# Optimization experiments

Measured on AMD Instinct MI355X. Metric: run time of the kernel, lower is better.

## Reference

```python
import jax, jax.numpy as jnp
import numpy as np

B, T, L, W = 4, 4096, 64, 8          # batch, text len, media tokens, max_window_per_audio
DIM, DIM_A, H, DH = 2048, 1024, 8, 64
INNER = H * DH
LN_EPS = 1e-5


def setup_inputs() -> dict:
    key = jax.random.key(0)
    ks = jax.random.split(key, 8)
    x = jax.random.normal(ks[0], (B, T, DIM), jnp.float32)
    media = jax.random.normal(ks[1], (B, L, 1, DIM_A), jnp.float32)
    media_mask = jax.random.uniform(ks[2], (B, L, 1)) > 0.1
    # sparse media markers (~8 per row); ensure at least one per row
    media_locations = (jax.random.uniform(ks[3], (B, T)) < (8.0 / T)).astype(jnp.int32)
    media_locations = media_locations.at[:, 0].set(1)
    Wq = jax.random.normal(ks[4], (DIM, INNER), jnp.float32) / np.sqrt(DIM).astype(np.float32)
    Wkv = jax.random.normal(ks[5], (DIM_A, 2 * INNER), jnp.float32) / np.sqrt(DIM_A).astype(np.float32)
    Wout = jax.random.normal(ks[6], (INNER, DIM), jnp.float32) / np.sqrt(INNER).astype(np.float32)
    gamma = jnp.ones((DIM,), jnp.float32)
    beta = jnp.zeros((DIM,), jnp.float32)
    return dict(x=x, media=media, media_mask=media_mask, media_locations=media_locations,
                Wq=Wq, Wkv=Wkv, Wout=Wout, gamma=gamma, beta=beta)


def reference(x, media, media_mask, media_locations, Wq, Wkv, Wout, gamma, beta):
    scale = DH ** -0.5
    # LayerNorm (biased variance, like torch)
    mu = x.mean(-1, keepdims=True)
    var = x.var(-1, keepdims=True)
    xn = (x - mu) * jax.lax.rsqrt(var + LN_EPS) * gamma + beta
    # projections
    q = (xn @ Wq).reshape(B, T, H, DH).transpose(0, 2, 1, 3) * scale   # [B,h,T,dh]
    kv = media.reshape(B, L, DIM_A) @ Wkv
    k, v = jnp.split(kv, 2, axis=-1)
    k = k.reshape(B, L, H, DH).transpose(0, 2, 1, 3)                   # [B,h,L,dh]
    v = v.reshape(B, L, H, DH).transpose(0, 2, 1, 3)
    sim = jnp.einsum('bhid,bhjd->bhij', q, k)                          # [B,h,T,L]
    big = jnp.finfo(sim.dtype).max
    # media validity mask
    mm = media_mask.reshape(B, 1, 1, L)
    sim = jnp.where(mm, sim, -big)
    # few-shot window mask (only_attend_immediate_media=False):
    # token t attends windows [0, max(#media at <=t, 1) * W)
    cum = jnp.cumsum((media_locations != 0).astype(jnp.int32), axis=1)  # [B,T]
    end = jnp.maximum(cum, 1) * W                                       # [B,T]
    fsm = jnp.arange(L)[None, None, :] < end[:, :, None]                # [B,T,L]
    sim = jnp.where(fsm[:, None], sim, -big)
    sim = sim - jax.lax.stop_gradient(sim.max(-1, keepdims=True))
    attn = jax.nn.softmax(sim, axis=-1)
    out = jnp.einsum('bhij,bhjd->bhid', attn, v)                        # [B,h,T,dh]
    out = out.transpose(0, 2, 1, 3).reshape(B, T, INNER)
    return out @ Wout
```

## Files before the change

### kernel.cpp

```cpp
#include <hip/hip_runtime.h>
#include <float.h>

typedef __bf16 bf16;
typedef __bf16 bf16x8 __attribute__((ext_vector_type(8)));
typedef float f32x4 __attribute__((ext_vector_type(4)));

#define GAS __attribute__((address_space(1)))
#define LAS __attribute__((address_space(3)))

__device__ __forceinline__ void gload_lds16(const void* g, void* l) {
  __builtin_amdgcn_global_load_lds((const GAS unsigned int*)g, (LAS unsigned int*)l, 16, 0, 0);
}

template <int OUT_BF16>
__global__ __launch_bounds__(512, 2) void gemm_big(
    const bf16* __restrict__ A, const bf16* __restrict__ Bt,
    void* __restrict__ Cv, int M, int N, int K) {
  __shared__ __align__(16) bf16 Abuf[3][256 * 64];
  __shared__ __align__(16) bf16 Bbuf[3][128 * 64];
  const int tid = threadIdx.x, lane = tid & 63;
  const int w = tid >> 6, wr = w >> 2, wc = w & 3;
  const int g = lane >> 4, fr = lane & 15;

  const int gx = gridDim.x;
  const int nwg = gx * gridDim.y;
  int lid = blockIdx.y * gx + blockIdx.x;
  {
    const int qq = nwg >> 3, rr = nwg & 7;
    const int xcd = lid & 7, pos = lid >> 3;
    lid = (xcd < rr ? xcd * (qq + 1) : rr * (qq + 1) + (xcd - rr) * qq) + pos;
  }
  const int bx = lid % gx, by = lid / gx;
  const size_t m0 = (size_t)by * 256, n0 = (size_t)bx * 128;

  const int nt = K >> 6;
  const int srow = tid >> 3;
  const int sslot = tid & 7;

  f32x4 acc[8][2] = {};

  auto stage = [&](int t) {
    const int s = t % 3;
    const int kt = t << 6;
#pragma unroll
    for (int c = 0; c < 4; ++c) {
      const int r = c * 64 + srow;
      gload_lds16(A + (m0 + r) * (size_t)K + kt + ((sslot ^ (r & 7)) << 3),
                  &Abuf[s][c * 4096 + w * 512]);
    }
#pragma unroll
    for (int c = 0; c < 2; ++c) {
      const int r = c * 64 + srow;
      gload_lds16(Bt + (n0 + r) * (size_t)K + kt + ((sslot ^ (r & 7)) << 3),
                  &Bbuf[s][c * 4096 + w * 512]);
    }
  };

  auto rdA = [&](int s, int mi, int ks) {
    const int r = wr * 128 + mi * 16 + fr;
    return *(const bf16x8*)&Abuf[s][r * 64 + ((((ks << 2) | g) ^ (r & 7)) << 3)];
  };
  auto rdB = [&](int s, int ni, int ks) {
    const int r = wc * 32 + ni * 16 + fr;
    return *(const bf16x8*)&Bbuf[s][r * 64 + ((((ks << 2) | g) ^ (r & 7)) << 3)];
  };

  auto compute = [&](int t) {
    const int s = t % 3;
    bf16x8 bv[2][2];
#pragma unroll
    for (int ni = 0; ni < 2; ++ni)
#pragma unroll
      for (int ks = 0; ks < 2; ++ks) bv[ni][ks] = rdB(s, ni, ks);
    __builtin_amdgcn_s_setprio(1);
#pragma unroll
    for (int mi = 0; mi < 8; ++mi)
#pragma unroll
      for (int ks = 0; ks < 2; ++ks) {
        const bf16x8 av = rdA(s, mi, ks);
#pragma unroll
        for (int ni = 0; ni < 2; ++ni)
          acc[mi][ni] = __builtin_amdgcn_mfma_f32_16x16x32_bf16(
              av, bv[ni][ks], acc[mi][ni], 0, 0, 0);
      }
    __builtin_amdgcn_s_setprio(0);
  };

  stage(0);
  stage(1);

  for (int t = 0; t < nt - 1; ++t) {
    __builtin_amdgcn_sched_barrier(0);
    asm volatile("s_waitcnt vmcnt(6)" ::: "memory");
    __builtin_amdgcn_s_barrier();
    __builtin_amdgcn_sched_barrier(0);
    if (t + 2 < nt) stage(t + 2);
    compute(t);
  }
  __builtin_amdgcn_sched_barrier(0);
  asm volatile("s_waitcnt vmcnt(0)" ::: "memory");
  __builtin_amdgcn_s_barrier();
  __builtin_amdgcn_sched_barrier(0);
  compute(nt - 1);

#pragma unroll
  for (int mi = 0; mi < 8; ++mi)
#pragma unroll
    for (int ni = 0; ni < 2; ++ni)
#pragma unroll
      for (int rg = 0; rg < 4; ++rg) {
        const size_t row = m0 + wr * 128 + mi * 16 + g * 4 + rg;
        const size_t col = n0 + wc * 32 + ni * 16 + fr;
        if (OUT_BF16)
          ((bf16*)Cv)[row * (size_t)N + col] = (bf16)acc[mi][ni][rg];
        else
          ((float*)Cv)[row * (size_t)N + col] = acc[mi][ni][rg];
      }
}

template <int OUT_BF16>
__global__ __launch_bounds__(256, 2) void gemm_bt(
    const bf16* __restrict__ A, const bf16* __restrict__ Bt,
    void* __restrict__ Cv, int M, int N, int K) {
  __shared__ bf16 As[128 * 32];
  __shared__ bf16 Bs[128 * 32];
  const int tid = threadIdx.x;
  const int lane = tid & 63, w = tid >> 6;
  const int wr = w >> 1, wc = w & 1;

  const int gx = gridDim.x;
  const int nwg = gx * gridDim.y;
  int lid = blockIdx.y * gx + blockIdx.x;
  {
    const int qq = nwg >> 3, rr = nwg & 7;
    const int xcd = lid & 7, pos = lid >> 3;
    lid = (xcd < rr ? xcd * (qq + 1) : rr * (qq + 1) + (xcd - rr) * qq) + pos;
  }
  const int bx = lid % gx, by = lid / gx;
  const size_t m0 = (size_t)by * 128, n0 = (size_t)bx * 128;

  const int srow = lane >> 2, sslot = lane & 3;
  const int g = lane >> 4, fr = lane & 15;

  f32x4 acc[4][4] = {};

  for (int kt = 0; kt < K; kt += 32) {
    __syncthreads();
#pragma unroll
    for (int j = 0; j < 2; ++j) {
      const int c = 2 * w + j;
      const int r = c * 16 + srow;
      const int ks = (sslot ^ (r & 3)) << 3;
      gload_lds16(A + (m0 + r) * K + kt + ks, &As[c * 512]);
      gload_lds16(Bt + (n0 + r) * K + kt + ks, &Bs[c * 512]);
    }
    __syncthreads();
    bf16x8 av[4], bv[4];
#pragma unroll
    for (int mi = 0; mi < 4; ++mi) {
      const int r = wr * 64 + mi * 16 + fr;
      av[mi] = *(const bf16x8*)&As[r * 32 + ((g ^ (r & 3)) << 3)];
    }
#pragma unroll
    for (int ni = 0; ni < 4; ++ni) {
      const int r = wc * 64 + ni * 16 + fr;
      bv[ni] = *(const bf16x8*)&Bs[r * 32 + ((g ^ (r & 3)) << 3)];
    }
#pragma unroll
    for (int mi = 0; mi < 4; ++mi)
#pragma unroll
      for (int ni = 0; ni < 4; ++ni)
        acc[mi][ni] = __builtin_amdgcn_mfma_f32_16x16x32_bf16(
            av[mi], bv[ni], acc[mi][ni], 0, 0, 0);
  }

#pragma unroll
  for (int mi = 0; mi < 4; ++mi)
#pragma unroll
    for (int ni = 0; ni < 4; ++ni)
#pragma unroll
      for (int rg = 0; rg < 4; ++rg) {
        const size_t row = m0 + wr * 64 + mi * 16 + g * 4 + rg;
        const size_t col = n0 + wc * 64 + ni * 16 + fr;
        if (OUT_BF16)
          ((bf16*)Cv)[row * (size_t)N + col] = (bf16)acc[mi][ni][rg];
        else
          ((float*)Cv)[row * (size_t)N + col] = acc[mi][ni][rg];
      }
}

__device__ __forceinline__ void transp64(const float* __restrict__ src,
                                         bf16* __restrict__ dst, int R, int C,
                                         float scale, int tile, float* lds) {
  const int tilesC = C >> 6;
  const int tr = tile / tilesC, tc = tile % tilesC;
  const int r0 = tr << 6, c0 = tc << 6;
  const int tid = threadIdx.x;
  const int lr = tid >> 6, lc = tid & 63;
#pragma unroll
  for (int j = 0; j < 16; ++j) {
    const int r = j * 4 + lr;
    lds[r * 65 + lc] = src[(size_t)(r0 + r) * C + c0 + lc];
  }
  __syncthreads();
#pragma unroll
  for (int j = 0; j < 16; ++j) {
    const int rr = j * 4 + lr;
    dst[(size_t)(c0 + rr) * R + r0 + lc] = (bf16)(lds[lc * 65 + rr] * scale);
  }
}

__global__ __launch_bounds__(256) void prep_all(
    const float* __restrict__ x, const float* __restrict__ gamma,
    const float* __restrict__ beta, bf16* __restrict__ xn,
    const float* __restrict__ Wq, bf16* __restrict__ wqT,
    const float* __restrict__ Wkv, bf16* __restrict__ wkvT,
    const float* __restrict__ Wout, bf16* __restrict__ woT,
    const float* __restrict__ media, bf16* __restrict__ medb,
    const int* __restrict__ mloc, int* __restrict__ endw,
    const unsigned char* __restrict__ mraw, int* __restrict__ mk) {
  __shared__ float shf[64 * 65];
  const int blk = blockIdx.x, tid = threadIdx.x;

  if (blk < 16384) {
    const size_t base = (size_t)blk * 2048 + tid * 8;
    f32x4 v0 = *(const f32x4*)(x + base);
    f32x4 v1 = *(const f32x4*)(x + base + 4);
    float s = 0.f, q2 = 0.f;
#pragma unroll
    for (int j = 0; j < 4; ++j) {
      s += v0[j] + v1[j];
      q2 += v0[j] * v0[j] + v1[j] * v1[j];
    }
    for (int off = 32; off > 0; off >>= 1) {
      s += __shfl_down(s, off);
      q2 += __shfl_down(q2, off);
    }
    const int lane = tid & 63, wv = tid >> 6;
    if (lane == 0) { shf[wv] = s; shf[4 + wv] = q2; }
    __syncthreads();
    s = shf[0] + shf[1] + shf[2] + shf[3];
    q2 = shf[4] + shf[5] + shf[6] + shf[7];
    const float mu = s * (1.f / 2048.f);
    const float var = q2 * (1.f / 2048.f) - mu * mu;
    const float rs = rsqrtf(var + 1e-5f);
    f32x4 g0 = *(const f32x4*)(gamma + tid * 8);
    f32x4 g1 = *(const f32x4*)(gamma + tid * 8 + 4);
    f32x4 b0 = *(const f32x4*)(beta + tid * 8);
    f32x4 b1 = *(const f32x4*)(beta + tid * 8 + 4);
    bf16x8 o;
#pragma unroll
    for (int j = 0; j < 4; ++j) {
      o[j] = (bf16)((v0[j] - mu) * rs * g0[j] + b0[j]);
      o[4 + j] = (bf16)((v1[j] - mu) * rs * g1[j] + b1[j]);
    }
    *(bf16x8*)(xn + base) = o;
  } else if (blk < 16640) {
    transp64(Wq, wqT, 2048, 512, 0.125f, blk - 16384, shf);
  } else if (blk < 16896) {
    transp64(Wkv, wkvT, 1024, 1024, 1.f, blk - 16640, shf);
  } else if (blk < 17152) {
    transp64(Wout, woT, 512, 2048, 1.f, blk - 16896, shf);
  } else if (blk < 18176) {
    const int i = (blk - 17152) * 256 + tid;
    medb[i] = (bf16)media[i];
  } else if (blk < 18180) {
    int* part = (int*)shf;
    const int b = blk - 18176;
    int loc[16];
    int s = 0;
    const int base = b * 4096 + tid * 16;
#pragma unroll
    for (int j = 0; j < 16; ++j) {
      loc[j] = (mloc[base + j] != 0) ? 1 : 0;
      s += loc[j];
    }
    part[tid] = s;
    __syncthreads();
    for (int off = 1; off < 256; off <<= 1) {
      int v = (tid >= off) ? part[tid - off] : 0;
      __syncthreads();
      part[tid] += v;
      __syncthreads();
    }
    int c = (tid > 0) ? part[tid - 1] : 0;
#pragma unroll
    for (int j = 0; j < 16; ++j) {
      c += loc[j];
      int e = (c > 1 ? c : 1) << 3;
      endw[base + j] = e > 64 ? 64 : e;
    }
  } else {
    int* isbool = (int*)shf;
    if (tid == 0) *isbool = 0;
    __syncthreads();
    const unsigned char v = mraw[tid];
    if ((tid & 3) != 0 && v != 0) atomicOr(isbool, 1);
    __syncthreads();
    mk[tid] = (*isbool) ? (int)mraw[tid] : ((const int*)mraw)[tid];
  }
}

__global__ __launch_bounds__(256, 2) void attn_kernel(
    const bf16* __restrict__ q, const bf16* __restrict__ kv,
    const int* __restrict__ mk, const int* __restrict__ endw,
    bf16* __restrict__ ao) {
  __shared__ bf16 Ks[64 * 64], Vs[64 * 64], Ps[64 * 64];
  __shared__ int mks[64];
  const int tid = threadIdx.x, lane = tid & 63, w = tid >> 6;
  const int b = blockIdx.z, h = blockIdx.y, t0 = blockIdx.x * 64;

#pragma unroll
  for (int s0 = 0; s0 < 2; ++s0) {
    const int sidx = s0 * 256 + tid;
    const int r = sidx >> 3, sl = sidx & 7;
    *(bf16x8*)&Ks[r * 64 + ((sl ^ (r & 7)) << 3)] =
        *(const bf16x8*)&kv[(size_t)(b * 64 + r) * 1024 + h * 64 + sl * 8];
    bf16x8 vv =
        *(const bf16x8*)&kv[(size_t)(b * 64 + r) * 1024 + 512 + h * 64 + sl * 8];
#pragma unroll
    for (int j = 0; j < 8; ++j) {
      const int dh = sl * 8 + j;
      Vs[dh * 64 + ((((r >> 3) ^ (dh & 7)) << 3) | (r & 7))] = vv[j];
    }
  }
  if (tid < 64) mks[tid] = mk[b * 64 + tid];
  __syncthreads();

  const int g = lane >> 4, fr = lane & 15;
  bf16x8 aq[2];
#pragma unroll
  for (int kg = 0; kg < 2; ++kg)
    aq[kg] = *(const bf16x8*)&q[(size_t)(b * 4096 + t0 + w * 16 + fr) * 512 +
                                h * 64 + kg * 32 + g * 8];
  f32x4 sacc[4] = {};
#pragma unroll
  for (int kg = 0; kg < 2; ++kg)
#pragma unroll
    for (int ni = 0; ni < 4; ++ni) {
      const int r = ni * 16 + fr;
      bf16x8 bk = *(const bf16x8*)&Ks[r * 64 + (((kg * 4 + g) ^ (r & 7)) << 3)];
      sacc[ni] = __builtin_amdgcn_mfma_f32_16x16x32_bf16(aq[kg], bk, sacc[ni],
                                                         0, 0, 0);
    }

  const int4 ev4 = *(const int4*)&endw[b * 4096 + t0 + w * 16 + g * 4];
  const int ev[4] = {ev4.x, ev4.y, ev4.z, ev4.w};
  float p[4][4];
#pragma unroll
  for (int ni = 0; ni < 4; ++ni) {
    const int l = ni * 16 + fr;
    const bool mv = (mks[l] != 0);
#pragma unroll
    for (int rg = 0; rg < 4; ++rg)
      p[ni][rg] = (mv && (l < ev[rg])) ? sacc[ni][rg] : -FLT_MAX;
  }
#pragma unroll
  for (int rg = 0; rg < 4; ++rg) {
    float m = fmaxf(fmaxf(p[0][rg], p[1][rg]), fmaxf(p[2][rg], p[3][rg]));
    m = fmaxf(m, __shfl_xor(m, 1));
    m = fmaxf(m, __shfl_xor(m, 2));
    m = fmaxf(m, __shfl_xor(m, 4));
    m = fmaxf(m, __shfl_xor(m, 8));
    float sum = 0.f;
#pragma unroll
    for (int ni = 0; ni < 4; ++ni) {
      p[ni][rg] = __expf(p[ni][rg] - m);
      sum += p[ni][rg];
    }
    sum += __shfl_xor(sum, 1);
    sum += __shfl_xor(sum, 2);
    sum += __shfl_xor(sum, 4);
    sum += __shfl_xor(sum, 8);
    const float inv = 1.f / sum;
#pragma unroll
    for (int ni = 0; ni < 4; ++ni) p[ni][rg] *= inv;
  }
#pragma unroll
  for (int ni = 0; ni < 4; ++ni) {
    const int l = ni * 16 + fr;
#pragma unroll
    for (int rg = 0; rg < 4; ++rg) {
      const int tr = w * 16 + g * 4 + rg;
      Ps[tr * 64 + ((((l >> 3) ^ (tr & 7)) << 3) | (l & 7))] = (bf16)p[ni][rg];
    }
  }
  __syncthreads();

  bf16x8 pa[2];
#pragma unroll
  for (int kg = 0; kg < 2; ++kg) {
    const int r = w * 16 + fr;
    pa[kg] = *(const bf16x8*)&Ps[r * 64 + (((kg * 4 + g) ^ (r & 7)) << 3)];
  }
  f32x4 oacc[4] = {};
#pragma unroll
  for (int kg = 0; kg < 2; ++kg)
#pragma unroll
    for (int ni = 0; ni < 4; ++ni) {
      const int r = ni * 16 + fr;
      bf16x8 bv = *(const bf16x8*)&Vs[r * 64 + (((kg * 4 + g) ^ (r & 7)) << 3)];
      oacc[ni] = __builtin_amdgcn_mfma_f32_16x16x32_bf16(pa[kg], bv, oacc[ni],
                                                         0, 0, 0);
    }
#pragma unroll
  for (int ni = 0; ni < 4; ++ni)
#pragma unroll
    for (int rg = 0; rg < 4; ++rg)
      ao[(size_t)(b * 4096 + t0 + w * 16 + g * 4 + rg) * 512 + h * 64 +
         ni * 16 + fr] = (bf16)oacc[ni][rg];
}

extern "C" void kernel_launch(void* const* d_in, const int* in_sizes, int n_in,
                              void* d_out, int out_size, void* d_ws,
                              size_t ws_size, hipStream_t stream) {
  const float* x = (const float*)d_in[0];
  const float* media = (const float*)d_in[1];
  const unsigned char* mraw = (const unsigned char*)d_in[2];
  const int* mloc = (const int*)d_in[3];
  const float* Wq = (const float*)d_in[4];
  const float* Wkv = (const float*)d_in[5];
  const float* Wout = (const float*)d_in[6];
  const float* gamma = (const float*)d_in[7];
  const float* beta = (const float*)d_in[8];
  float* out = (float*)d_out;

  bf16* xn = (bf16*)d_out;

  char* ws = (char*)d_ws;
  size_t off = 0;
  auto carve = [&](size_t bytes) {
    void* p = ws + off;
    off += (bytes + 255) & ~(size_t)255;
    return p;
  };
  bf16* qb = (bf16*)carve((size_t)16384 * 512 * 2);
  bf16* aob = (bf16*)carve((size_t)16384 * 512 * 2);
  bf16* kvb = (bf16*)carve((size_t)256 * 1024 * 2);
  bf16* wqT = (bf16*)carve((size_t)512 * 2048 * 2);
  bf16* wkvT = (bf16*)carve((size_t)1024 * 1024 * 2);
  bf16* woT = (bf16*)carve((size_t)2048 * 512 * 2);
  bf16* medb = (bf16*)carve((size_t)256 * 1024 * 2);
  int* endw = (int*)carve((size_t)4 * 4096 * 4);
  int* mk = (int*)carve(256 * 4);
  (void)ws_size;
  (void)in_sizes;
  (void)n_in;
  (void)out_size;

  prep_all<<<18181, 256, 0, stream>>>(x, gamma, beta, xn, Wq, wqT, Wkv, wkvT,
                                      Wout, woT, media, medb, mloc, endw, mraw,
                                      mk);

  gemm_bt<1><<<dim3(8, 2), 256, 0, stream>>>(medb, wkvT, kvb, 256, 1024, 1024);

  gemm_big<1><<<dim3(4, 64), 512, 0, stream>>>(xn, wqT, qb, 16384, 512, 2048);

  attn_kernel<<<dim3(64, 8, 4), 256, 0, stream>>>(qb, kvb, mk, endw, aob);

  gemm_big<0><<<dim3(16, 64), 512, 0, stream>>>(aob, woT, out, 16384, 2048,
                                                512);
}
```

Baseline: 182.4 us.

## Replace big GEMM with 4-stage K=32 pipeline interleaving loads between MFMA phases

```diff
diff --git a/kernel.cpp b/kernel.cpp
--- a/kernel.cpp
+++ b/kernel.cpp
@@ -12,14 +12,30 @@
   __builtin_amdgcn_global_load_lds((const GAS unsigned int*)g, (LAS unsigned int*)l, 16, 0, 0);
 }
 
-template <int OUT_BF16>
-__global__ __launch_bounds__(512, 2) void gemm_big(
+template <int N> struct ic { static constexpr int v = N; };
+
+template <int VM> __device__ __forceinline__ void wait_vmcnt() {
+  if constexpr (VM == 0) asm volatile("s_waitcnt vmcnt(0)" ::: "memory");
+  else if constexpr (VM == 3) asm volatile("s_waitcnt vmcnt(3)" ::: "memory");
+  else if constexpr (VM == 4) asm volatile("s_waitcnt vmcnt(4)" ::: "memory");
+  else if constexpr (VM == 6) asm volatile("s_waitcnt vmcnt(6)" ::: "memory");
+  else if constexpr (VM == 8) asm volatile("s_waitcnt vmcnt(8)" ::: "memory");
+  else if constexpr (VM == 10) asm volatile("s_waitcnt vmcnt(10)" ::: "memory");
+}
+
+template <int OUT_BF16, int BN, int WM, int WN>
+__global__ __launch_bounds__(512, 2) void gemm_8ph(
     const bf16* __restrict__ A, const bf16* __restrict__ Bt,
     void* __restrict__ Cv, int M, int N, int K) {
-  __shared__ __align__(16) bf16 Abuf[3][256 * 64];
-  __shared__ __align__(16) bf16 Bbuf[3][128 * 64];
+  constexpr int M_rep = 256 / WM / 16;
+  constexpr int VMAIN = (BN == 256) ? 10 : 8;
+  constexpr int VP0 = (BN == 256) ? 8 : 6;
+  constexpr int VP1 = (BN == 256) ? 4 : 3;
+  __shared__ __align__(16) bf16 Ab[4][256 * 32];
+  __shared__ __align__(16) bf16 Bb[4][BN * 32];
+
   const int tid = threadIdx.x, lane = tid & 63;
-  const int w = tid >> 6, wr = w >> 2, wc = w & 3;
+  const int w = tid >> 6, wr = w / WN, wc = w % WN;
   const int g = lane >> 4, fr = lane & 15;
 
   const int gx = gridDim.x;
@@ -31,86 +47,101 @@
     lid = (xcd < rr ? xcd * (qq + 1) : rr * (qq + 1) + (xcd - rr) * qq) + pos;
   }
   const int bx = lid % gx, by = lid / gx;
-  const size_t m0 = (size_t)by * 256, n0 = (size_t)bx * 128;
-
-  const int nt = K >> 6;
-  const int srow = tid >> 3;
-  const int sslot = tid & 7;
-
-  f32x4 acc[8][2] = {};
-
-  auto stage = [&](int t) {
-    const int s = t % 3;
-    const int kt = t << 6;
-#pragma unroll
-    for (int c = 0; c < 4; ++c) {
-      const int r = c * 64 + srow;
-      gload_lds16(A + (m0 + r) * (size_t)K + kt + ((sslot ^ (r & 7)) << 3),
-                  &Abuf[s][c * 4096 + w * 512]);
-    }
+  const size_t m0 = (size_t)by * 256, n0 = (size_t)bx * BN;
+
+  const int ns = K >> 5;
+  const int srow = tid >> 2, sslot = tid & 3;
+
+  auto stageA = [&](int s) {
+    const int b4 = s & 3, kt = s << 5;
 #pragma unroll
     for (int c = 0; c < 2; ++c) {
-      const int r = c * 64 + srow;
-      gload_lds16(Bt + (n0 + r) * (size_t)K + kt + ((sslot ^ (r & 7)) << 3),
-                  &Bbuf[s][c * 4096 + w * 512]);
-    }
-  };
-
-  auto rdA = [&](int s, int mi, int ks) {
-    const int r = wr * 128 + mi * 16 + fr;
-    return *(const bf16x8*)&Abuf[s][r * 64 + ((((ks << 2) | g) ^ (r & 7)) << 3)];
-  };
-  auto rdB = [&](int s, int ni, int ks) {
-    const int r = wc * 32 + ni * 16 + fr;
-    return *(const bf16x8*)&Bbuf[s][r * 64 + ((((ks << 2) | g) ^ (r & 7)) << 3)];
-  };
-
-  auto compute = [&](int t) {
-    const int s = t % 3;
-    bf16x8 bv[2][2];
-#pragma unroll
-    for (int ni = 0; ni < 2; ++ni)
-#pragma unroll
-      for (int ks = 0; ks < 2; ++ks) bv[ni][ks] = rdB(s, ni, ks);
+      const int r = c * 128 + srow;
+      gload_lds16(A + (m0 + r) * (size_t)K + kt + ((sslot ^ (r & 3)) << 3),
+                  &Ab[b4][c * 4096 + tid * 8]);
+    }
+  };
+  auto stageB = [&](int s) {
+    const int b4 = s & 3, kt = s << 5;
+#pragma unroll
+    for (int c = 0; c < BN / 128; ++c) {
+      const int r = c * 128 + srow;
+      gload_lds16(Bt + (n0 + r) * (size_t)K + kt + ((sslot ^ (r & 3)) << 3),
+                  &Bb[b4][c * 4096 + tid * 8]);
+    }
+  };
+  auto rdA = [&](int b4, int mi) {
+    const int r = wr * (256 / WM) + mi * 16 + fr;
+    return *(const bf16x8*)&Ab[b4][r * 32 + ((g ^ (r & 3)) << 3)];
+  };
+  auto rdB = [&](int b4, int ni) {
+    const int r = wc * 64 + ni * 16 + fr;
+    return *(const bf16x8*)&Bb[b4][r * 32 + ((g ^ (r & 3)) << 3)];
+  };
+
+  f32x4 acc[M_rep][4] = {};
+
+  auto subtile = [&](int s, auto vmtag, bool doStage) {
+    const int b4 = s & 3;
+    bf16x8 av[M_rep], bv0, bv1;
+    if (doStage) stageA(s + 3);
+    wait_vmcnt<decltype(vmtag)::v>();
+    __builtin_amdgcn_s_barrier();
+    __builtin_amdgcn_sched_barrier(0);
+#pragma unroll
+    for (int mi = 0; mi < M_rep; ++mi) av[mi] = rdA(b4, mi);
+    bv0 = rdB(b4, 0);
+    bv1 = rdB(b4, 1);
+    asm volatile("s_waitcnt lgkmcnt(0)" ::: "memory");
+    __builtin_amdgcn_sched_barrier(0);
     __builtin_amdgcn_s_setprio(1);
 #pragma unroll
-    for (int mi = 0; mi < 8; ++mi)
-#pragma unroll
-      for (int ks = 0; ks < 2; ++ks) {
-        const bf16x8 av = rdA(s, mi, ks);
-#pragma unroll
-        for (int ni = 0; ni < 2; ++ni)
-          acc[mi][ni] = __builtin_amdgcn_mfma_f32_16x16x32_bf16(
-              av, bv[ni][ks], acc[mi][ni], 0, 0, 0);
-      }
+    for (int mi = 0; mi < M_rep; ++mi) {
+      acc[mi][0] = __builtin_amdgcn_mfma_f32_16x16x32_bf16(av[mi], bv0,
+                                                           acc[mi][0], 0, 0, 0);
+      acc[mi][1] = __builtin_amdgcn_mfma_f32_16x16x32_bf16(av[mi], bv1,
+                                                           acc[mi][1], 0, 0, 0);
+    }
     __builtin_amdgcn_s_setprio(0);
-  };
-
-  stage(0);
-  stage(1);
-
-  for (int t = 0; t < nt - 1; ++t) {
-    __builtin_amdgcn_sched_barrier(0);
-    asm volatile("s_waitcnt vmcnt(6)" ::: "memory");
     __builtin_amdgcn_s_barrier();
     __builtin_amdgcn_sched_barrier(0);
-    if (t + 2 < nt) stage(t + 2);
-    compute(t);
-  }
-  __builtin_amdgcn_sched_barrier(0);
-  asm volatile("s_waitcnt vmcnt(0)" ::: "memory");
-  __builtin_amdgcn_s_barrier();
-  __builtin_amdgcn_sched_barrier(0);
-  compute(nt - 1);
-
-#pragma unroll
-  for (int mi = 0; mi < 8; ++mi)
-#pragma unroll
-    for (int ni = 0; ni < 2; ++ni)
+    if (doStage) stageB(s + 3);
+    __builtin_amdgcn_s_barrier();
+    __builtin_amdgcn_sched_barrier(0);
+    bv0 = rdB(b4, 2);
+    bv1 = rdB(b4, 3);
+    asm volatile("s_waitcnt lgkmcnt(0)" ::: "memory");
+    __builtin_amdgcn_sched_barrier(0);
+    __builtin_amdgcn_s_setprio(1);
+#pragma unroll
+    for (int mi = 0; mi < M_rep; ++mi) {
+      acc[mi][2] = __builtin_amdgcn_mfma_f32_16x16x32_bf16(av[mi], bv0,
+                                                           acc[mi][2], 0, 0, 0);
+      acc[mi][3] = __builtin_amdgcn_mfma_f32_16x16x32_bf16(av[mi], bv1,
+                                                           acc[mi][3], 0, 0, 0);
+    }
+    __builtin_amdgcn_s_setprio(0);
+    __builtin_amdgcn_s_barrier();
+    __builtin_amdgcn_sched_barrier(0);
+  };
+
+  stageA(0); stageB(0);
+  stageA(1); stageB(1);
+  stageA(2); stageB(2);
+
+  for (int s = 0; s < ns - 3; ++s) subtile(s, ic<VMAIN>{}, true);
+  subtile(ns - 3, ic<VP0>{}, false);
+  subtile(ns - 2, ic<VP1>{}, false);
+  subtile(ns - 1, ic<0>{}, false);
+
+#pragma unroll
+  for (int mi = 0; mi < M_rep; ++mi)
+#pragma unroll
+    for (int ni = 0; ni < 4; ++ni)
 #pragma unroll
       for (int rg = 0; rg < 4; ++rg) {
-        const size_t row = m0 + wr * 128 + mi * 16 + g * 4 + rg;
-        const size_t col = n0 + wc * 32 + ni * 16 + fr;
+        const size_t row = m0 + wr * (256 / WM) + mi * 16 + g * 4 + rg;
+        const size_t col = n0 + wc * 64 + ni * 16 + fr;
         if (OUT_BF16)
           ((bf16*)Cv)[row * (size_t)N + col] = (bf16)acc[mi][ni][rg];
         else
@@ -454,10 +485,11 @@
 
   gemm_bt<1><<<dim3(8, 2), 256, 0, stream>>>(medb, wkvT, kvb, 256, 1024, 1024);
 
-  gemm_big<1><<<dim3(4, 64), 512, 0, stream>>>(xn, wqT, qb, 16384, 512, 2048);
+  gemm_8ph<1, 128, 4, 2><<<dim3(4, 64), 512, 0, stream>>>(xn, wqT, qb, 16384,
+                                                          512, 2048);
 
   attn_kernel<<<dim3(64, 8, 4), 256, 0, stream>>>(qb, kvb, mk, endw, aob);
 
-  gemm_big<0><<<dim3(16, 64), 512, 0, stream>>>(aob, woT, out, 16384, 2048,
-                                                512);
-}
+  gemm_8ph<0, 256, 2, 4><<<dim3(8, 64), 512, 0, stream>>>(aob, woT, out, 16384,
+                                                          2048, 512);
+}
```

Measured after the change: 202.3 us. +10.9%, slower.
